# Optimization experiments

Measured on AMD Instinct MI355X. Metric: run time of the kernel, lower is better.

## Reference

```python
import jax, jax.numpy as jnp
import numpy as np

B, S, IN_F, OUT_F = 8, 2048, 2048, 2048
ORDER, RANK, LEAF = 3, 4, 13  # LEAF = ceil(IN_F ** (1/ORDER))


def setup_inputs() -> dict:
    key = jax.random.key(0)
    k1, k2, k3, k4 = jax.random.split(key, 4)
    inp = jax.random.normal(k1, (B, S, IN_F), dtype=jnp.float32)
    # leaf init ~ uniform(-std, std), std = gain / in_features**(1/order)
    gain = float(np.sqrt(2.0 / (1.0 + 5.0)))  # leaky_relu gain with param=sqrt(5)
    std = gain / (IN_F ** (1.0 / ORDER))
    leaf_tensor = jax.random.uniform(k2, (ORDER, RANK, LEAF, LEAF), dtype=jnp.float32,
                                     minval=-std, maxval=std)
    bound = 1.0 / np.sqrt(IN_F)
    weight = jax.random.uniform(k3, (OUT_F, IN_F), dtype=jnp.float32, minval=-bound, maxval=bound)
    bias = jax.random.uniform(k4, (OUT_F,), dtype=jnp.float32, minval=-bound, maxval=bound)
    return {"input": inp, "leaf_tensor": leaf_tensor, "weight": weight, "bias": bias}


def tensor_product_represent(leaf_tensor, out_dim, in_dim):
    order, rank, leaf, _ = leaf_tensor.shape  # static shapes
    base = leaf_tensor[0]                      # [rank, leaf, leaf]
    dim = leaf
    for i in range(1, order):                  # fixed small structural loop
        # Kronecker step: [r, d, d] x [r, l, l] -> [r, d*l, d*l]
        base = jnp.einsum('abc,ade->abdce', base, leaf_tensor[i])
        dim = dim * leaf
        base = base.reshape(rank, dim, dim)
    base = base.sum(axis=0)                    # [leaf^order, leaf^order]
    return base[:out_dim, :in_dim]


def reference(input, leaf_tensor, weight, bias):
    out_dim, in_dim = weight.shape
    delta = tensor_product_represent(leaf_tensor, out_dim, in_dim)
    w = weight + delta                          # [out, in]
    # F.linear: y = x @ w.T + b
    return jnp.einsum('bsi,oi->bso', input, w) + bias
```

## Files before the change

kernel.cpp:

```cpp
#include <hip/hip_runtime.h>
#include <hip/hip_bf16.h>
#include <stdint.h>

#define MROWS 16384
#define KDIM  2048
#define NDIM  2048
#define LEAFD 13
#define RANKD 4

typedef __bf16 bf16x8 __attribute__((ext_vector_type(8)));
typedef float  f32x4  __attribute__((ext_vector_type(4)));
typedef float  f32x16 __attribute__((ext_vector_type(16)));

__global__ void build_w_kernel(const float* __restrict__ weight,
                               const float* __restrict__ leaf,
                               __hip_bfloat16* __restrict__ wbf) {
    __shared__ float ll[3 * RANKD * LEAFD * LEAFD];
    for (int t = threadIdx.x; t < 3 * RANKD * LEAFD * LEAFD; t += blockDim.x)
        ll[t] = leaf[t];
    __syncthreads();
    int idx = blockIdx.x * blockDim.x + threadIdx.x;
    if (idx >= NDIM * KDIM) return;
    int o = idx / KDIM, i = idx % KDIM;
    int o2 = o / 169, o1 = (o / 13) % 13, o0 = o % 13;
    int i2 = i / 169, i1 = (i / 13) % 13, i0 = i % 13;
    float d = 0.f;
#pragma unroll
    for (int r = 0; r < RANKD; ++r) {
        float a = ll[( r            * LEAFD + o2) * LEAFD + i2];
        float b = ll[((RANKD   + r) * LEAFD + o1) * LEAFD + i1];
        float c = ll[((2*RANKD + r) * LEAFD + o0) * LEAFD + i0];
        d += a * b * c;
    }
    wbf[idx] = __float2bfloat16(weight[idx] + d);
}

__global__ void cvt_kernel(const float* __restrict__ x,
                           __hip_bfloat16* __restrict__ xb, int n) {
    long stride = (long)gridDim.x * blockDim.x * 8;
    for (long idx = ((long)blockIdx.x * blockDim.x + threadIdx.x) * 8; idx < n; idx += stride) {
        float4 v0 = *reinterpret_cast<const float4*>(x + idx);
        float4 v1 = *reinterpret_cast<const float4*>(x + idx + 4);
        __hip_bfloat16 tmp[8];
        tmp[0] = __float2bfloat16(v0.x); tmp[1] = __float2bfloat16(v0.y);
        tmp[2] = __float2bfloat16(v0.z); tmp[3] = __float2bfloat16(v0.w);
        tmp[4] = __float2bfloat16(v1.x); tmp[5] = __float2bfloat16(v1.y);
        tmp[6] = __float2bfloat16(v1.z); tmp[7] = __float2bfloat16(v1.w);
        *reinterpret_cast<uint4*>(xb + idx) = *reinterpret_cast<const uint4*>(tmp);
    }
}


__device__ __forceinline__ void gload16(const __hip_bfloat16* g, char* l) {
    __builtin_amdgcn_global_load_lds((const __attribute__((address_space(1))) void*)g,
                                     (__attribute__((address_space(3))) void*)l,
                                     16, 0, 0);
}

#define STAGE(base, kb, bufi, slot) do {                                          \
    gload16((base) + (kb) + gOff0, smemc + (bufi)*32768 + (slot)*16384 + lOff0);  \
    gload16((base) + (kb) + gOff1, smemc + (bufi)*32768 + (slot)*16384 + lOff1);  \
} while (0)

#define LOADK(ks, bufc)                                                       \
    a0 = *(const bf16x8*)(smemc + (bufc)*32768 + offA[0][ks]);                \
    a1 = *(const bf16x8*)(smemc + (bufc)*32768 + offA[1][ks]);                \
    a2 = *(const bf16x8*)(smemc + (bufc)*32768 + offA[2][ks]);                \
    a3 = *(const bf16x8*)(smemc + (bufc)*32768 + offA[3][ks]);                \
    b0 = *(const bf16x8*)(smemc + (bufc)*32768 + 16384 + offB[0][ks]);        \
    b1 = *(const bf16x8*)(smemc + (bufc)*32768 + 16384 + offB[1][ks]);

#define MFMA8 do {                                                                  \
    acc[0][0] = __builtin_amdgcn_mfma_f32_32x32x16_bf16(a0, b0, acc[0][0], 0,0,0);  \
    acc[1][0] = __builtin_amdgcn_mfma_f32_32x32x16_bf16(a1, b0, acc[1][0], 0,0,0);  \
    acc[2][0] = __builtin_amdgcn_mfma_f32_32x32x16_bf16(a2, b0, acc[2][0], 0,0,0);  \
    acc[3][0] = __builtin_amdgcn_mfma_f32_32x32x16_bf16(a3, b0, acc[3][0], 0,0,0);  \
    acc[0][1] = __builtin_amdgcn_mfma_f32_32x32x16_bf16(a0, b1, acc[0][1], 0,0,0);  \
    acc[1][1] = __builtin_amdgcn_mfma_f32_32x32x16_bf16(a1, b1, acc[1][1], 0,0,0);  \
    acc[2][1] = __builtin_amdgcn_mfma_f32_32x32x16_bf16(a2, b1, acc[2][1], 0,0,0);  \
    acc[3][1] = __builtin_amdgcn_mfma_f32_32x32x16_bf16(a3, b1, acc[3][1], 0,0,0);  \
} while (0)

#define BARRIER_IN do {                                     \
    __builtin_amdgcn_sched_barrier(0);                      \
    __builtin_amdgcn_s_barrier();                           \
    asm volatile("s_waitcnt lgkmcnt(0)" ::: "memory");      \
    __builtin_amdgcn_sched_barrier(0);                      \
    __builtin_amdgcn_s_setprio(1);                          \
} while (0)

#define BARRIER_OUT do {                                    \
    __builtin_amdgcn_s_setprio(0);                          \
    __builtin_amdgcn_sched_barrier(0);                      \
    __builtin_amdgcn_s_barrier();                           \
    __builtin_amdgcn_sched_barrier(0);                      \
} while (0)

#define WAIT4 asm volatile("s_waitcnt vmcnt(4)" ::: "memory")
#define WAIT0 asm volatile("s_waitcnt vmcnt(0)" ::: "memory")
#define WNONE do {} while (0)

#define KTILE3(t, bufc, bufs, SG, WT) do {                          \
    LOADK(0, bufc);                                                 \
    if (SG) { STAGE(Abase, ((t)+2)*32, bufs, 0);                    \
              STAGE(Bbase, ((t)+2)*32, bufs, 1); }                  \
    BARRIER_IN;                                                     \
    MFMA8;                                                          \
    LOADK(1, bufc);                                                 \
    asm volatile("s_waitcnt lgkmcnt(0)" ::: "memory");              \
    __builtin_amdgcn_sched_barrier(0);                              \
    MFMA8;                                                          \
    WT;                                                             \
    BARRIER_OUT;                                                    \
} while (0)

__global__ __launch_bounds__(512, 2) void gemm3_kernel(const __hip_bfloat16* __restrict__ A,
                                                       const __hip_bfloat16* __restrict__ Wb,
                                                       const float* __restrict__ bias,
                                                       float* __restrict__ C) {
    __shared__ __align__(16) __hip_bfloat16 smem[3][2][8192];
    char* smemc = (char*)&smem[0][0][0];

    const int tid  = threadIdx.x;
    const int lane = tid & 63;
    const int wid  = tid >> 6;
    const int wr   = wid >> 2;
    const int wc   = wid & 3;

    const int bid = blockIdx.x;
    const int swz = (bid & 7) * 64 + (bid >> 3);
    const int bn  = swz >> 6;
    const int bm  = swz & 63;

    const __hip_bfloat16* Abase = A  + (size_t)bm * 256 * KDIM;
    const __hip_bfloat16* Bbase = Wb + (size_t)bn * 256 * KDIM;

    const int c0  = wid * 64 + lane;
    const int c1  = 512 + wid * 64 + lane;
    const int cs0 = c0 ^ ((c0 >> 3) & 7);
    const int cs1 = c1 ^ ((c1 >> 3) & 7);
    const int gOff0 = (cs0 >> 2) * KDIM + (cs0 & 3) * 8;
    const int gOff1 = (cs1 >> 2) * KDIM + (cs1 & 3) * 8;
    const int lOff0 = wid * 1024;
    const int lOff1 = 8192 + wid * 1024;

    const int l31 = lane & 31;
    const int kh  = (lane >> 5) * 16;
    int offA[4][2], offB[2][2];
#pragma unroll
    for (int mf = 0; mf < 4; ++mf)
#pragma unroll
        for (int ks = 0; ks < 2; ++ks) {
            int a = (wr * 128 + mf * 32 + l31) * 64 + ks * 32 + kh;
            offA[mf][ks] = a ^ (((a >> 7) & 7) << 4);
        }
#pragma unroll
    for (int nf = 0; nf < 2; ++nf)
#pragma unroll
        for (int ks = 0; ks < 2; ++ks) {
            int a = (wc * 64 + nf * 32 + l31) * 64 + ks * 32 + kh;
            offB[nf][ks] = a ^ (((a >> 7) & 7) << 4);
        }

    f32x16 acc[4][2];
#pragma unroll
    for (int mf = 0; mf < 4; ++mf)
#pragma unroll
        for (int nf = 0; nf < 2; ++nf)
#pragma unroll
            for (int r = 0; r < 16; ++r)
                acc[mf][nf][r] = 0.f;

    bf16x8 a0, a1, a2, a3, b0, b1;

    STAGE(Abase,  0, 0, 0);
    STAGE(Bbase,  0, 0, 1);
    STAGE(Abase, 32, 1, 0);
    STAGE(Bbase, 32, 1, 1);
    WAIT4;
    __builtin_amdgcn_sched_barrier(0);
    __builtin_amdgcn_s_barrier();
    __builtin_amdgcn_sched_barrier(0);

    for (int t = 0; t < 60; t += 3) {
        KTILE3(t,     0, 2, 1, WAIT4);
        KTILE3(t + 1, 1, 0, 1, WAIT4);
        KTILE3(t + 2, 2, 1, 1, WAIT4);
    }
    KTILE3(60, 0, 2, 1, WAIT4);
    KTILE3(61, 1, 0, 1, WAIT4);
    KTILE3(62, 2, 1, 0, WAIT0);
    KTILE3(63, 0, 1, 0, WNONE);

    const int rupper = 4 * (lane >> 5);
#pragma unroll
    for (int nf = 0; nf < 2; ++nf) {
        const int cg = bn * 256 + wc * 64 + nf * 32 + l31;
        const float bv = bias[cg];
#pragma unroll
        for (int mf = 0; mf < 4; ++mf) {
            const size_t rb = (size_t)bm * 256 + wr * 128 + mf * 32 + rupper;
#pragma unroll
            for (int reg = 0; reg < 16; ++reg) {
                const int row = (reg & 3) + 8 * (reg >> 2);
                C[(rb + row) * NDIM + cg] = acc[mf][nf][reg] + bv;
            }
        }
    }
}

__global__ void naive_kernel(const float* __restrict__ x,
                             const float* __restrict__ leaf,
                             const float* __restrict__ W,
                             const float* __restrict__ bias,
                             float* __restrict__ out) {
    long idx = (long)blockIdx.x * blockDim.x + threadIdx.x;
    if (idx >= (long)MROWS * NDIM) return;
    int  o = (int)(idx % NDIM);
    long m = idx / NDIM;
    int o2 = o / 169, o1 = (o / 13) % 13, o0 = o % 13;
    float acc = 0.f;
    for (int i = 0; i < KDIM; ++i) {
        int i2 = i / 169, i1 = (i / 13) % 13, i0 = i % 13;
        float d = 0.f;
#pragma unroll
        for (int r = 0; r < RANKD; ++r)
            d += leaf[( r     * LEAFD + o2) * LEAFD + i2]
               * leaf[((4 + r) * LEAFD + o1) * LEAFD + i1]
               * leaf[((8 + r) * LEAFD + o0) * LEAFD + i0];
        acc += x[m * KDIM + i] * (W[(long)o * KDIM + i] + d);
    }
    out[idx] = acc + bias[o];
}

extern "C" void kernel_launch(void* const* d_in, const int* in_sizes, int n_in,
                              void* d_out, int out_size, void* d_ws, size_t ws_size,
                              hipStream_t stream) {
    const float* x      = (const float*)d_in[0];
    const float* leaf   = (const float*)d_in[1];
    const float* weight = (const float*)d_in[2];
    const float* bias   = (const float*)d_in[3];
    float* out = (float*)d_out;

    const size_t needA = (size_t)MROWS * KDIM * sizeof(__hip_bfloat16);
    const size_t needW = (size_t)NDIM  * KDIM * sizeof(__hip_bfloat16);

    if (ws_size >= needA + needW) {
        __hip_bfloat16* xb = (__hip_bfloat16*)d_ws;
        __hip_bfloat16* wb = (__hip_bfloat16*)((char*)d_ws + needA);
        build_w_kernel<<<(NDIM * KDIM + 255) / 256, 256, 0, stream>>>(weight, leaf, wb);
        cvt_kernel<<<2048, 256, 0, stream>>>(x, xb, MROWS * KDIM);
        gemm3_kernel<<<(MROWS / 256) * (NDIM / 256), 512, 0, stream>>>(xb, wb, bias, out);
    } else {
        long total = (long)MROWS * NDIM;
        naive_kernel<<<(int)((total + 255) / 256), 256, 0, stream>>>(x, leaf, weight, bias, out);
    }
}
```

Baseline: 209.7 us.

## Deepen GEMM LDS pipeline to four stages with register double-buffered fragments

Replaces the three-buffer GEMM mainloop with a four-stage LDS ring and prefetches the next tile's first k-slice into a second register set while the current tile's MFMAs run. This cuts the loop to one barrier per tile instead of two, and the global-to-LDS swizzle and the LDS read offsets are reworked to match. LDS use per block grows to 128 KB, which may limit occupancy against the requested two blocks per CU, and the extra fragment registers raise register pressure.

```diff
diff --git a/kernel.cpp b/kernel.cpp
--- a/kernel.cpp
+++ b/kernel.cpp
@@ -9,7 +9,6 @@
 #define RANKD 4
 
 typedef __bf16 bf16x8 __attribute__((ext_vector_type(8)));
-typedef float  f32x4  __attribute__((ext_vector_type(4)));
 typedef float  f32x16 __attribute__((ext_vector_type(16)));
 
 __global__ void build_w_kernel(const float* __restrict__ weight,
@@ -57,69 +56,81 @@
                                      16, 0, 0);
 }
 
-#define STAGE(base, kb, bufi, slot) do {                                          \
-    gload16((base) + (kb) + gOff0, smemc + (bufi)*32768 + (slot)*16384 + lOff0);  \
-    gload16((base) + (kb) + gOff1, smemc + (bufi)*32768 + (slot)*16384 + lOff1);  \
-} while (0)
-
-#define LOADK(ks, bufc)                                                       \
-    a0 = *(const bf16x8*)(smemc + (bufc)*32768 + offA[0][ks]);                \
-    a1 = *(const bf16x8*)(smemc + (bufc)*32768 + offA[1][ks]);                \
-    a2 = *(const bf16x8*)(smemc + (bufc)*32768 + offA[2][ks]);                \
-    a3 = *(const bf16x8*)(smemc + (bufc)*32768 + offA[3][ks]);                \
-    b0 = *(const bf16x8*)(smemc + (bufc)*32768 + 16384 + offB[0][ks]);        \
-    b1 = *(const bf16x8*)(smemc + (bufc)*32768 + 16384 + offB[1][ks]);
-
-#define MFMA8 do {                                                                  \
-    acc[0][0] = __builtin_amdgcn_mfma_f32_32x32x16_bf16(a0, b0, acc[0][0], 0,0,0);  \
-    acc[1][0] = __builtin_amdgcn_mfma_f32_32x32x16_bf16(a1, b0, acc[1][0], 0,0,0);  \
-    acc[2][0] = __builtin_amdgcn_mfma_f32_32x32x16_bf16(a2, b0, acc[2][0], 0,0,0);  \
-    acc[3][0] = __builtin_amdgcn_mfma_f32_32x32x16_bf16(a3, b0, acc[3][0], 0,0,0);  \
-    acc[0][1] = __builtin_amdgcn_mfma_f32_32x32x16_bf16(a0, b1, acc[0][1], 0,0,0);  \
-    acc[1][1] = __builtin_amdgcn_mfma_f32_32x32x16_bf16(a1, b1, acc[1][1], 0,0,0);  \
-    acc[2][1] = __builtin_amdgcn_mfma_f32_32x32x16_bf16(a2, b1, acc[2][1], 0,0,0);  \
-    acc[3][1] = __builtin_amdgcn_mfma_f32_32x32x16_bf16(a3, b1, acc[3][1], 0,0,0);  \
-} while (0)
-
-#define BARRIER_IN do {                                     \
-    __builtin_amdgcn_sched_barrier(0);                      \
-    __builtin_amdgcn_s_barrier();                           \
-    asm volatile("s_waitcnt lgkmcnt(0)" ::: "memory");      \
-    __builtin_amdgcn_sched_barrier(0);                      \
-    __builtin_amdgcn_s_setprio(1);                          \
-} while (0)
-
-#define BARRIER_OUT do {                                    \
-    __builtin_amdgcn_s_setprio(0);                          \
-    __builtin_amdgcn_sched_barrier(0);                      \
-    __builtin_amdgcn_s_barrier();                           \
-    __builtin_amdgcn_sched_barrier(0);                      \
-} while (0)
-
+#define SB __builtin_amdgcn_sched_barrier(0)
 #define WAIT4 asm volatile("s_waitcnt vmcnt(4)" ::: "memory")
 #define WAIT0 asm volatile("s_waitcnt vmcnt(0)" ::: "memory")
 #define WNONE do {} while (0)
 
-#define KTILE3(t, bufc, bufs, SG, WT) do {                          \
-    LOADK(0, bufc);                                                 \
-    if (SG) { STAGE(Abase, ((t)+2)*32, bufs, 0);                    \
-              STAGE(Bbase, ((t)+2)*32, bufs, 1); }                  \
-    BARRIER_IN;                                                     \
-    MFMA8;                                                          \
-    LOADK(1, bufc);                                                 \
-    asm volatile("s_waitcnt lgkmcnt(0)" ::: "memory");              \
-    __builtin_amdgcn_sched_barrier(0);                              \
-    MFMA8;                                                          \
-    WT;                                                             \
-    BARRIER_OUT;                                                    \
-} while (0)
-
-__global__ __launch_bounds__(512, 2) void gemm3_kernel(const __hip_bfloat16* __restrict__ A,
+#define STAGEPAIR(KB, BS) do {                                                  \
+    gload16(Abase + (KB) + gOff0, smemc + (BS)*32768 + lOff0);                  \
+    gload16(Abase + (KB) + gOff1, smemc + (BS)*32768 + lOff1);                  \
+    gload16(Bbase + (KB) + gOff0, smemc + (BS)*32768 + 16384 + lOff0);          \
+    gload16(Bbase + (KB) + gOff1, smemc + (BS)*32768 + 16384 + lOff1);          \
+} while (0)
+
+#define RD(off) (*(const bf16x8*)(smemc + (off)))
+
+#define MFMA8R(A0,A1,A2,A3,B0,B1) do {                                              \
+    acc00 = __builtin_amdgcn_mfma_f32_32x32x16_bf16(A0, B0, acc00, 0,0,0);          \
+    acc10 = __builtin_amdgcn_mfma_f32_32x32x16_bf16(A1, B0, acc10, 0,0,0);          \
+    acc20 = __builtin_amdgcn_mfma_f32_32x32x16_bf16(A2, B0, acc20, 0,0,0);          \
+    acc30 = __builtin_amdgcn_mfma_f32_32x32x16_bf16(A3, B0, acc30, 0,0,0);          \
+    acc01 = __builtin_amdgcn_mfma_f32_32x32x16_bf16(A0, B1, acc01, 0,0,0);          \
+    acc11 = __builtin_amdgcn_mfma_f32_32x32x16_bf16(A1, B1, acc11, 0,0,0);          \
+    acc21 = __builtin_amdgcn_mfma_f32_32x32x16_bf16(A2, B1, acc21, 0,0,0);          \
+    acc31 = __builtin_amdgcn_mfma_f32_32x32x16_bf16(A3, B1, acc31, 0,0,0);          \
+} while (0)
+
+#define TILE(BC, BN, BS, KB, SG, WT, A0,A1,A2,A3,B0,B1, N0,N1,N2,N3,M0,M1) do { \
+    if (SG) STAGEPAIR(KB, BS);                                                  \
+    SB;                                                                         \
+    __builtin_amdgcn_s_setprio(1);                                              \
+    MFMA8R(A0,A1,A2,A3,B0,B1);                                                  \
+    __builtin_amdgcn_s_setprio(0);                                              \
+    SB;                                                                         \
+    c0 = RD((BC)*32768 + aB + 0*2048 + lk1);                                    \
+    c1 = RD((BC)*32768 + aB + 1*2048 + lk1);                                    \
+    c2 = RD((BC)*32768 + aB + 2*2048 + lk1);                                    \
+    c3 = RD((BC)*32768 + aB + 3*2048 + lk1);                                    \
+    d0 = RD((BC)*32768 + bB + 0*2048 + lk1);                                    \
+    d1 = RD((BC)*32768 + bB + 1*2048 + lk1);                                    \
+    N0 = RD((BN)*32768 + aB + 0*2048 + lk0);                                    \
+    N1 = RD((BN)*32768 + aB + 1*2048 + lk0);                                    \
+    N2 = RD((BN)*32768 + aB + 2*2048 + lk0);                                    \
+    N3 = RD((BN)*32768 + aB + 3*2048 + lk0);                                    \
+    M0 = RD((BN)*32768 + bB + 0*2048 + lk0);                                    \
+    M1 = RD((BN)*32768 + bB + 1*2048 + lk0);                                    \
+    SB;                                                                         \
+    __builtin_amdgcn_s_setprio(1);                                              \
+    MFMA8R(c0,c1,c2,c3,d0,d1);                                                  \
+    __builtin_amdgcn_s_setprio(0);                                              \
+    WT;                                                                         \
+    SB;                                                                         \
+    __builtin_amdgcn_s_barrier();                                               \
+    SB;                                                                         \
+} while (0)
+
+#define TILE_LAST(BC, A0,A1,A2,A3,B0,B1) do {                                   \
+    __builtin_amdgcn_s_setprio(1);                                              \
+    MFMA8R(A0,A1,A2,A3,B0,B1);                                                  \
+    __builtin_amdgcn_s_setprio(0);                                              \
+    c0 = RD((BC)*32768 + aB + 0*2048 + lk1);                                    \
+    c1 = RD((BC)*32768 + aB + 1*2048 + lk1);                                    \
+    c2 = RD((BC)*32768 + aB + 2*2048 + lk1);                                    \
+    c3 = RD((BC)*32768 + aB + 3*2048 + lk1);                                    \
+    d0 = RD((BC)*32768 + bB + 0*2048 + lk1);                                    \
+    d1 = RD((BC)*32768 + bB + 1*2048 + lk1);                                    \
+    __builtin_amdgcn_s_setprio(1);                                              \
+    MFMA8R(c0,c1,c2,c3,d0,d1);                                                  \
+    __builtin_amdgcn_s_setprio(0);                                              \
+} while (0)
+
+__global__ __launch_bounds__(512, 2) void gemm4_kernel(const __hip_bfloat16* __restrict__ A,
                                                        const __hip_bfloat16* __restrict__ Wb,
                                                        const float* __restrict__ bias,
                                                        float* __restrict__ C) {
-    __shared__ __align__(16) __hip_bfloat16 smem[3][2][8192];
-    char* smemc = (char*)&smem[0][0][0];
+    __shared__ __align__(16) __hip_bfloat16 smem[4][2][8192];
+    char* smemc = (char*)smem;
 
     const int tid  = threadIdx.x;
     const int lane = tid & 63;
@@ -135,64 +146,57 @@
     const __hip_bfloat16* Abase = A  + (size_t)bm * 256 * KDIM;
     const __hip_bfloat16* Bbase = Wb + (size_t)bn * 256 * KDIM;
 
-    const int c0  = wid * 64 + lane;
-    const int c1  = 512 + wid * 64 + lane;
-    const int cs0 = c0 ^ ((c0 >> 3) & 7);
-    const int cs1 = c1 ^ ((c1 >> 3) & 7);
-    const int gOff0 = (cs0 >> 2) * KDIM + (cs0 & 3) * 8;
-    const int gOff1 = (cs1 >> 2) * KDIM + (cs1 & 3) * 8;
+    const int r16   = wid * 16 + (lane >> 2);
+    const int slt   = (lane & 3) ^ ((lane >> 3) & 3);
+    const int gOff0 = r16 * KDIM + slt * 8;
+    const int gOff1 = gOff0 + 128 * KDIM;
     const int lOff0 = wid * 1024;
     const int lOff1 = 8192 + wid * 1024;
 
     const int l31 = lane & 31;
-    const int kh  = (lane >> 5) * 16;
-    int offA[4][2], offB[2][2];
-#pragma unroll
-    for (int mf = 0; mf < 4; ++mf)
-#pragma unroll
-        for (int ks = 0; ks < 2; ++ks) {
-            int a = (wr * 128 + mf * 32 + l31) * 64 + ks * 32 + kh;
-            offA[mf][ks] = a ^ (((a >> 7) & 7) << 4);
-        }
-#pragma unroll
-    for (int nf = 0; nf < 2; ++nf)
-#pragma unroll
-        for (int ks = 0; ks < 2; ++ks) {
-            int a = (wc * 64 + nf * 32 + l31) * 64 + ks * 32 + kh;
-            offB[nf][ks] = a ^ (((a >> 7) & 7) << 4);
-        }
-
-    f32x16 acc[4][2];
-#pragma unroll
-    for (int mf = 0; mf < 4; ++mf)
-#pragma unroll
-        for (int nf = 0; nf < 2; ++nf)
-#pragma unroll
-            for (int r = 0; r < 16; ++r)
-                acc[mf][nf][r] = 0.f;
-
-    bf16x8 a0, a1, a2, a3, b0, b1;
-
-    STAGE(Abase,  0, 0, 0);
-    STAGE(Bbase,  0, 0, 1);
-    STAGE(Abase, 32, 1, 0);
-    STAGE(Bbase, 32, 1, 1);
-    WAIT4;
-    __builtin_amdgcn_sched_barrier(0);
-    __builtin_amdgcn_s_barrier();
-    __builtin_amdgcn_sched_barrier(0);
-
-    for (int t = 0; t < 60; t += 3) {
-        KTILE3(t,     0, 2, 1, WAIT4);
-        KTILE3(t + 1, 1, 0, 1, WAIT4);
-        KTILE3(t + 2, 2, 1, 1, WAIT4);
-    }
-    KTILE3(60, 0, 2, 1, WAIT4);
-    KTILE3(61, 1, 0, 1, WAIT4);
-    KTILE3(62, 2, 1, 0, WAIT0);
-    KTILE3(63, 0, 1, 0, WNONE);
-
-    const int rupper = 4 * (lane >> 5);
+    const int h   = lane >> 5;
+    const int lk0 = l31 * 64 + (((0 * 2 + h) ^ ((l31 >> 1) & 3)) << 4);
+    const int lk1 = l31 * 64 + (((1 * 2 + h) ^ ((l31 >> 1) & 3)) << 4);
+    const int aB  = wr * 8192;
+    const int bB  = 16384 + wc * 4096;
+
+    f32x16 acc00{}, acc10{}, acc20{}, acc30{}, acc01{}, acc11{}, acc21{}, acc31{};
+
+    bf16x8 aE0, aE1, aE2, aE3, bE0, bE1;
+    bf16x8 aO0, aO1, aO2, aO3, bO0, bO1;
+    bf16x8 c0, c1, c2, c3, d0, d1;
+
+    STAGEPAIR( 0, 0);
+    STAGEPAIR(32, 1);
+    STAGEPAIR(64, 2);
+    asm volatile("s_waitcnt vmcnt(8)" ::: "memory");
+    SB; __builtin_amdgcn_s_barrier(); SB;
+    aE0 = RD(aB + 0*2048 + lk0);
+    aE1 = RD(aB + 1*2048 + lk0);
+    aE2 = RD(aB + 2*2048 + lk0);
+    aE3 = RD(aB + 3*2048 + lk0);
+    bE0 = RD(bB + 0*2048 + lk0);
+    bE1 = RD(bB + 1*2048 + lk0);
+    asm volatile("s_waitcnt vmcnt(4)" ::: "memory");
+    SB; __builtin_amdgcn_s_barrier(); SB;
+
+    for (int t = 0; t < 56; t += 4) {
+        TILE(0, 1, 3, (t+3)*32, 1, WAIT4, aE0,aE1,aE2,aE3,bE0,bE1, aO0,aO1,aO2,aO3,bO0,bO1);
+        TILE(1, 2, 0, (t+4)*32, 1, WAIT4, aO0,aO1,aO2,aO3,bO0,bO1, aE0,aE1,aE2,aE3,bE0,bE1);
+        TILE(2, 3, 1, (t+5)*32, 1, WAIT4, aE0,aE1,aE2,aE3,bE0,bE1, aO0,aO1,aO2,aO3,bO0,bO1);
+        TILE(3, 0, 2, (t+6)*32, 1, WAIT4, aO0,aO1,aO2,aO3,bO0,bO1, aE0,aE1,aE2,aE3,bE0,bE1);
+    }
+    TILE(0, 1, 3, 59*32, 1, WAIT4, aE0,aE1,aE2,aE3,bE0,bE1, aO0,aO1,aO2,aO3,bO0,bO1);
+    TILE(1, 2, 0, 60*32, 1, WAIT4, aO0,aO1,aO2,aO3,bO0,bO1, aE0,aE1,aE2,aE3,bE0,bE1);
+    TILE(2, 3, 1, 61*32, 1, WAIT4, aE0,aE1,aE2,aE3,bE0,bE1, aO0,aO1,aO2,aO3,bO0,bO1);
+    TILE(3, 0, 2, 62*32, 1, WAIT4, aO0,aO1,aO2,aO3,bO0,bO1, aE0,aE1,aE2,aE3,bE0,bE1);
+    TILE(0, 1, 3, 63*32, 1, WAIT4, aE0,aE1,aE2,aE3,bE0,bE1, aO0,aO1,aO2,aO3,bO0,bO1);
+    TILE(1, 2, 0, 0,     0, WAIT0, aO0,aO1,aO2,aO3,bO0,bO1, aE0,aE1,aE2,aE3,bE0,bE1);
+    TILE(2, 3, 1, 0,     0, WNONE, aE0,aE1,aE2,aE3,bE0,bE1, aO0,aO1,aO2,aO3,bO0,bO1);
+    TILE_LAST(3, aO0,aO1,aO2,aO3,bO0,bO1);
+
+    const int rupper = 4 * h;
+    f32x16* accp[4][2] = {{&acc00,&acc01},{&acc10,&acc11},{&acc20,&acc21},{&acc30,&acc31}};
 #pragma unroll
     for (int nf = 0; nf < 2; ++nf) {
         const int cg = bn * 256 + wc * 64 + nf * 32 + l31;
@@ -200,10 +204,11 @@
 #pragma unroll
         for (int mf = 0; mf < 4; ++mf) {
             const size_t rb = (size_t)bm * 256 + wr * 128 + mf * 32 + rupper;
+            const f32x16 av = *accp[mf][nf];
 #pragma unroll
             for (int reg = 0; reg < 16; ++reg) {
                 const int row = (reg & 3) + 8 * (reg >> 2);
-                C[(rb + row) * NDIM + cg] = acc[mf][nf][reg] + bv;
+                C[(rb + row) * NDIM + cg] = av[reg] + bv;
             }
         }
     }
@@ -250,7 +255,7 @@
         __hip_bfloat16* wb = (__hip_bfloat16*)((char*)d_ws + needA);
         build_w_kernel<<<(NDIM * KDIM + 255) / 256, 256, 0, stream>>>(weight, leaf, wb);
         cvt_kernel<<<2048, 256, 0, stream>>>(x, xb, MROWS * KDIM);
-        gemm3_kernel<<<(MROWS / 256) * (NDIM / 256), 512, 0, stream>>>(xb, wb, bias, out);
+        gemm4_kernel<<<(MROWS / 256) * (NDIM / 256), 512, 0, stream>>>(xb, wb, bias, out);
     } else {
         long total = (long)MROWS * NDIM;
         naive_kernel<<<(int)((total + 255) / 256), 256, 0, stream>>>(x, leaf, weight, bias, out);
```

Result: no change. 211.2 us (+0.7%).
